# Kernel optimization log

Hardware: AMD Instinct MI355X
Metric: run time of the kernel (lower is better)

Reference implementation:

```python
import jax, jax.numpy as jnp
import numpy as np

DIM = 1024
HEADS = 16
DIM_HEAD = DIM // HEADS  # 64
MAX_FREQ = 256


def rotate_half(x):
    # interleaved pairs: (..., d) -> rotate each (x1, x2) pair to (-x2, x1)
    x = x.reshape(*x.shape[:-1], -1, 2)
    x1, x2 = x[..., 0], x[..., 1]
    return jnp.stack([-x2, x1], axis=-1).reshape(*x.shape[:-2], -1)


def axial_freqs_2d(H, W, rot_dim, max_freq):
    # 'pixel' freqs: linspace(1, max_freq/2, n) * pi per axis; each axis gets rot_dim/2 rotary dims
    n = rot_dim // 4
    freqs = jnp.linspace(1.0, max_freq / 2.0, n, dtype=jnp.float32) * jnp.pi
    ph = jnp.linspace(-1.0, 1.0, H, dtype=jnp.float32)
    pw = jnp.linspace(-1.0, 1.0, W, dtype=jnp.float32)
    fh = jnp.repeat(ph[:, None] * freqs[None, :], 2, axis=-1)  # (H, rot_dim//2)
    fw = jnp.repeat(pw[:, None] * freqs[None, :], 2, axis=-1)  # (W, rot_dim//2)
    fh = jnp.broadcast_to(fh[:, None, :], (H, W, rot_dim // 2))
    fw = jnp.broadcast_to(fw[None, :, :], (H, W, rot_dim // 2))
    return jnp.concatenate([fh, fw], axis=-1)  # (H, W, rot_dim)


def setup_inputs() -> dict:
    key = jax.random.key(0)
    k1, k2, k3 = jax.random.split(key, 3)
    b, H, W = 8, 32, 32
    L = H * W
    x = jax.random.normal(k1, (b, L, DIM), dtype=jnp.float32)
    # torch Linear weights stored pre-transposed for direct x @ W
    w_qkv = jax.random.normal(k2, (DIM, 3 * DIM), dtype=jnp.float32) * (DIM ** -0.5)
    w_proj = jax.random.normal(k3, (DIM, DIM), dtype=jnp.float32) * (DIM ** -0.5)
    return {"x": x, "w_qkv": w_qkv, "w_proj": w_proj, "H": H, "W": W}


def reference(x, w_qkv, w_proj, H, W):
    b, L, d = x.shape
    qkv = x @ w_qkv  # (b, L, 3d)
    q, k, v = jnp.split(qkv, 3, axis=-1)

    def split_heads(t):
        return t.reshape(b, L, HEADS, DIM_HEAD)  # (b, L, h, dh)

    q, k, v = split_heads(q), split_heads(k), split_heads(v)

    # 2D axial RoPE over the full head dim (rope_use_dim == dim_head)
    freqs = axial_freqs_2d(H, W, DIM_HEAD, MAX_FREQ).reshape(L, DIM_HEAD)
    cos = jnp.cos(freqs)[None, :, None, :]  # (1, L, 1, dh)
    sin = jnp.sin(freqs)[None, :, None, :]
    q = q * cos + rotate_half(q) * sin
    k = k * cos + rotate_half(k) * sin

    # module pre-scales q by dh^-0.5 AND SDPA scales again by dh^-0.5 -> dh^-1 total (faithful)
    scale_total = 1.0 / DIM_HEAD
    scores = jnp.einsum('blhd,bmhd->bhlm', q, k) * scale_total  # (b, h, L, L)
    attn = jax.nn.softmax(scores, axis=-1)
    out = jnp.einsum('bhlm,bmhd->blhd', attn, v).reshape(b, L, d)
    return out @ w_proj
```

## Files before the change

### kernel.cpp

```cpp
#include <hip/hip_runtime.h>
#include <hip/hip_bf16.h>
#include <math.h>

typedef __bf16 bf16_t;
typedef __attribute__((ext_vector_type(8))) __bf16 bf16x8;
typedef __attribute__((ext_vector_type(4))) __bf16 bf16x4;
typedef __attribute__((ext_vector_type(4))) short s16x4;
typedef __attribute__((ext_vector_type(4))) float f32x4;

#define AS1C(p) ((const __attribute__((address_space(1))) void*)(p))
#define AS3(p)  ((__attribute__((address_space(3))) void*)(p))

__device__ __forceinline__ float fast_exp2(float x) { return __builtin_amdgcn_exp2f(x); }

__global__ __launch_bounds__(256) void k_cvt(const float* __restrict__ in,
                                             bf16_t* __restrict__ out, int n4) {
    int i = blockIdx.x * 256 + threadIdx.x;
    if (i < n4) {
        float4 v = reinterpret_cast<const float4*>(in)[i];
        bf16x4 o;
        o[0] = (bf16_t)v.x; o[1] = (bf16_t)v.y; o[2] = (bf16_t)v.z; o[3] = (bf16_t)v.w;
        reinterpret_cast<bf16x4*>(out)[i] = o;
    }
}

__global__ __launch_bounds__(256) void k_tconv(const float* __restrict__ in,
                                               bf16_t* __restrict__ out, int R, int C) {
    __shared__ float tile[64][65];
    int r0 = blockIdx.y * 64, c0 = blockIdx.x * 64;
#pragma unroll
    for (int i = 0; i < 16; ++i) {
        int e = i * 256 + threadIdx.x;
        int r = e >> 6, c = e & 63;
        tile[r][c] = in[(size_t)(r0 + r) * C + c0 + c];
    }
    __syncthreads();
#pragma unroll
    for (int i = 0; i < 16; ++i) {
        int e = i * 256 + threadIdx.x;
        int c = e >> 6, r = e & 63;
        out[(size_t)(c0 + c) * R + r0 + r] = (bf16_t)tile[r][c];
    }
}

__global__ __launch_bounds__(256) void k_tab(float* __restrict__ cosT,
                                             float* __restrict__ sinT) {
    int i = blockIdx.x * 256 + threadIdx.x;
    int l = i >> 6, d = i & 63;
    int hh = l >> 5, ww = l & 31;
    float pos = (d < 32) ? (-1.0f + (2.0f / 31.0f) * (float)hh)
                         : (-1.0f + (2.0f / 31.0f) * (float)ww);
    int fi = (d & 31) >> 1;
    float fb = (1.0f + (127.0f / 15.0f) * (float)fi) * 3.14159265358979323846f;
    float fr = pos * fb;
    cosT[i] = cosf(fr);
    sinT[i] = sinf(fr);
}

__device__ __forceinline__ void gemm_core(const bf16_t* __restrict__ A,
                                          const bf16_t* __restrict__ Bt,
                                          int K, int rowA0, int colB0,
                                          int w, int l, bf16_t* As, bf16_t* Bs,
                                          f32x4 acc[4][4]) {
    const int wr = w >> 1, wc = w & 1;
    for (int kt = 0; kt < K; kt += 64) {
#pragma unroll
        for (int i = 0; i < 4; ++i) {
            int rr = (i * 4 + w) * 8 + (l >> 3);
            int ch = (l & 7) * 8;
            __builtin_amdgcn_global_load_lds(AS1C(A + (size_t)(rowA0 + rr) * K + kt + ch),
                                             AS3(As + (i * 4 + w) * 512), 16, 0, 0);
            __builtin_amdgcn_global_load_lds(AS1C(Bt + (size_t)(colB0 + rr) * K + kt + ch),
                                             AS3(Bs + (i * 4 + w) * 512), 16, 0, 0);
        }
        __syncthreads();
#pragma unroll
        for (int kk = 0; kk < 2; ++kk) {
            bf16x8 af[4], bfr[4];
#pragma unroll
            for (int m = 0; m < 4; ++m)
                af[m] = *reinterpret_cast<const bf16x8*>(
                    As + (wr * 64 + m * 16 + (l & 15)) * 64 + kk * 32 + (l >> 4) * 8);
#pragma unroll
            for (int n = 0; n < 4; ++n)
                bfr[n] = *reinterpret_cast<const bf16x8*>(
                    Bs + (wc * 64 + n * 16 + (l & 15)) * 64 + kk * 32 + (l >> 4) * 8);
#pragma unroll
            for (int m = 0; m < 4; ++m)
#pragma unroll
                for (int n = 0; n < 4; ++n)
                    acc[m][n] = __builtin_amdgcn_mfma_f32_16x16x32_bf16(af[m], bfr[n],
                                                                        acc[m][n], 0, 0, 0);
        }
        __syncthreads();
    }
}

__global__ __launch_bounds__(256) void k_gemm_qkv(const bf16_t* __restrict__ A,
                                                  const bf16_t* __restrict__ Bt,
                                                  const float* __restrict__ cosT,
                                                  const float* __restrict__ sinT,
                                                  bf16_t* __restrict__ qb,
                                                  bf16_t* __restrict__ kb,
                                                  bf16_t* __restrict__ vb) {
    __shared__ alignas(128) bf16_t As[128 * 64];
    __shared__ alignas(128) bf16_t Bs[128 * 64];
    const int tid = threadIdx.x, w = tid >> 6, l = tid & 63;
    const int rowA0 = blockIdx.y * 128, colB0 = blockIdx.x * 128;
    f32x4 acc[4][4] = {};
    gemm_core(A, Bt, 1024, rowA0, colB0, w, l, As, Bs, acc);
    const int wr = w >> 1, wc = w & 1;
    const int part = colB0 >> 10;
#pragma unroll
    for (int m = 0; m < 4; ++m) {
#pragma unroll
        for (int n = 0; n < 4; ++n) {
            const int c = colB0 + wc * 64 + n * 16 + (l & 15);
            const int head = (c & 1023) >> 6;
            const int d = c & 63;
            const int rbase = rowA0 + wr * 64 + m * 16 + (l >> 4) * 4;
            if (part == 2) {
#pragma unroll
                for (int r = 0; r < 4; ++r) {
                    int row = rbase + r;
                    int bb = row >> 10, ll = row & 1023;
                    vb[(((size_t)bb * 16 + head) * 64 + d) * 1024 + ll] = (bf16_t)acc[m][n][r];
                }
            } else {
                bf16_t* dst = (part == 0) ? qb : kb;
#pragma unroll
                for (int r = 0; r < 4; ++r) {
                    int row = rbase + r;
                    int bb = row >> 10, ll = row & 1023;
                    float v0 = acc[m][n][r];
                    float vp = __shfl_xor(v0, 1, 64);
                    float cs = cosT[ll * 64 + d];
                    float sn = sinT[ll * 64 + d];
                    float res = (d & 1) ? fmaf(vp, sn, v0 * cs) : fmaf(-vp, sn, v0 * cs);
                    dst[(((size_t)bb * 16 + head) * 1024 + ll) * 64 + d] = (bf16_t)res;
                }
            }
        }
    }
}

__global__ __launch_bounds__(256) void k_gemm_out(const bf16_t* __restrict__ A,
                                                  const bf16_t* __restrict__ Bt,
                                                  float* __restrict__ out) {
    __shared__ alignas(128) bf16_t As[128 * 64];
    __shared__ alignas(128) bf16_t Bs[128 * 64];
    const int tid = threadIdx.x, w = tid >> 6, l = tid & 63;
    const int rowA0 = blockIdx.y * 128, colB0 = blockIdx.x * 128;
    f32x4 acc[4][4] = {};
    gemm_core(A, Bt, 1024, rowA0, colB0, w, l, As, Bs, acc);
    const int wr = w >> 1, wc = w & 1;
#pragma unroll
    for (int m = 0; m < 4; ++m)
#pragma unroll
        for (int n = 0; n < 4; ++n) {
            int c = colB0 + wc * 64 + n * 16 + (l & 15);
            int rbase = rowA0 + wr * 64 + m * 16 + (l >> 4) * 4;
#pragma unroll
            for (int r = 0; r < 4; ++r)
                out[(size_t)(rbase + r) * 1024 + c] = acc[m][n][r];
        }
}

__global__ __launch_bounds__(256, 4) void k_attn(const bf16_t* __restrict__ qb,
                                                 const bf16_t* __restrict__ kb,
                                                 const bf16_t* __restrict__ vb,
                                                 bf16_t* __restrict__ ob) {
    __shared__ alignas(128) bf16_t Ks[2][64 * 64];
    __shared__ alignas(128) bf16_t Vs[2][64 * 64];
    const int tid = threadIdx.x, w = tid >> 6, l = tid & 63;
    const int g = l >> 4;
    const int bid = blockIdx.x;
    const int bs = (bid & 7) * 128 + (bid >> 3);
    const int bh = bs >> 3, bi = bh >> 4, h = bh & 15;
    const int q0 = (bs & 7) * 128;
    const bf16_t* qbase = qb + (size_t)bh * 1024 * 64;
    const bf16_t* kbase = kb + (size_t)bh * 1024 * 64;
    const bf16_t* vbase = vb + (size_t)bh * 64 * 1024;

    bf16x8 qf[2][2];
#pragma unroll
    for (int m = 0; m < 2; ++m) {
        int qrow = q0 + m * 64 + w * 16 + (l & 15);
#pragma unroll
        for (int kk = 0; kk < 2; ++kk)
            qf[m][kk] = *reinterpret_cast<const bf16x8*>(
                qbase + (size_t)qrow * 64 + kk * 32 + g * 8);
    }

    float m_run[2] = {-1e30f, -1e30f};
    float l_run[2] = {0.f, 0.f};
    f32x4 o_acc[2][4] = {};

    const int srow = l >> 3;
    const int sc = 8 * ((l & 7) ^ srow);
#define STAGE(buf, kv0)                                                                   \
    {                                                                                     \
        _Pragma("unroll")                                                                 \
        for (int i = 0; i < 2; ++i) {                                                     \
            int rr = (i * 4 + w) * 8 + srow;                                              \
            __builtin_amdgcn_global_load_lds(AS1C(kbase + (size_t)((kv0) + rr) * 64 + sc),\
                                             AS3(&Ks[buf][(i * 4 + w) * 512]), 16, 0, 0); \
            __builtin_amdgcn_global_load_lds(AS1C(vbase + (size_t)rr * 1024 + (kv0) + sc),\
                                             AS3(&Vs[buf][(i * 4 + w) * 512]), 16, 0, 0); \
        }                                                                                 \
    }

    STAGE(0, 0);
    __syncthreads();

    const float SCL = 1.4426950408889634f / 64.0f;
    int cur = 0;
    for (int t = 0; t < 16; ++t) {
        if (t < 15) STAGE(cur ^ 1, (t + 1) * 64);

        f32x4 sacc[2][4] = {};
#pragma unroll
        for (int kk = 0; kk < 2; ++kk)
#pragma unroll
            for (int n = 0; n < 4; ++n) {
                int rr = n * 16 + (l & 15);
                int ec = (kk * 32 + g * 8) ^ ((l & 7) << 3);
                bf16x8 kfr = *reinterpret_cast<const bf16x8*>(&Ks[cur][rr * 64 + ec]);
                sacc[0][n] = __builtin_amdgcn_mfma_f32_16x16x32_bf16(kfr, qf[0][kk], sacc[0][n], 0, 0, 0);
                sacc[1][n] = __builtin_amdgcn_mfma_f32_16x16x32_bf16(kfr, qf[1][kk], sacc[1][n], 0, 0, 0);
            }

        s16x4 pa[2][4];
#pragma unroll
        for (int m = 0; m < 2; ++m) {
            float mxr = -1e30f;
#pragma unroll
            for (int n = 0; n < 4; ++n)
#pragma unroll
                for (int r = 0; r < 4; ++r) mxr = fmaxf(mxr, sacc[m][n][r]);
            mxr = fmaxf(mxr, __shfl_xor(mxr, 16, 64));
            mxr = fmaxf(mxr, __shfl_xor(mxr, 32, 64));
            float mx = mxr * SCL;
            float mo = m_run[m];
            if (__any(mx > mo + 8.0f)) {
                float mn = fmaxf(mo, mx);
                float corr = fast_exp2(mo - mn);
                l_run[m] *= corr;
                m_run[m] = mn; mo = mn;
#pragma unroll
                for (int r = 0; r < 4; ++r) {
                    float c2 = __shfl(corr, (l & 48) | (g * 4 + r), 64);
#pragma unroll
                    for (int n = 0; n < 4; ++n) o_acc[m][n][r] *= c2;
                }
            }
            float lsum = 0.f;
#pragma unroll
            for (int n = 0; n < 4; ++n) {
                bf16x4 pb;
#pragma unroll
                for (int r = 0; r < 4; ++r) {
                    float pv = fast_exp2(fmaf(sacc[m][n][r], SCL, -mo));
                    lsum += pv;
                    pb[r] = (bf16_t)pv;
                }
                pa[m][n] = __builtin_bit_cast(s16x4, pb);
            }
            l_run[m] += lsum;
        }

        const char* vrow = (const char*)&Vs[cur][0] + (l & 15) * 128;
#pragma unroll
        for (int c = 0; c < 4; ++c) {
            int kvb = (c * 32 + g * 8) ^ ((l & 7) << 4);
#pragma unroll
            for (int nd = 0; nd < 4; ++nd) {
                s16x4 vf = *reinterpret_cast<const s16x4*>(vrow + nd * 2048 + kvb);
                o_acc[0][nd] = __builtin_amdgcn_mfma_f32_16x16x16bf16_1k(pa[0][c], vf, o_acc[0][nd], 0, 0, 0);
                o_acc[1][nd] = __builtin_amdgcn_mfma_f32_16x16x16bf16_1k(pa[1][c], vf, o_acc[1][nd], 0, 0, 0);
            }
        }
        __syncthreads();
        cur ^= 1;
    }

#pragma unroll
    for (int m = 0; m < 2; ++m) {
        float ls = l_run[m];
        ls += __shfl_xor(ls, 16, 64);
        ls += __shfl_xor(ls, 32, 64);
        float inv = 1.0f / ls;
#pragma unroll
        for (int r = 0; r < 4; ++r) {
            float c2 = __shfl(inv, (l & 48) | (g * 4 + r), 64);
            int row = q0 + m * 64 + w * 16 + g * 4 + r;
#pragma unroll
            for (int n = 0; n < 4; ++n)
                ob[((size_t)bi * 1024 + row) * 1024 + h * 64 + n * 16 + (l & 15)] =
                    (bf16_t)(o_acc[m][n][r] * c2);
        }
    }
#undef STAGE
}

extern "C" void kernel_launch(void* const* d_in, const int* in_sizes, int n_in,
                              void* d_out, int out_size, void* d_ws, size_t ws_size,
                              hipStream_t stream) {
    (void)in_sizes; (void)n_in; (void)out_size; (void)ws_size;
    const float* x     = (const float*)d_in[0];
    const float* wqkv  = (const float*)d_in[1];
    const float* wproj = (const float*)d_in[2];
    char* ws = (char*)d_ws;

    bf16_t* xb  = (bf16_t*)(ws);
    bf16_t* wqT = (bf16_t*)(ws + 16777216ull);
    bf16_t* wpT = (bf16_t*)(ws + 23068672ull);
    bf16_t* qb  = (bf16_t*)(ws + 25165824ull);
    bf16_t* kb  = (bf16_t*)(ws + 41943040ull);
    bf16_t* vb  = (bf16_t*)(ws + 58720256ull);
    bf16_t* ob  = (bf16_t*)(ws + 75497472ull);
    float*  cosT = (float*)(ws + 92274688ull);
    float*  sinT = (float*)(ws + 92536832ull);

    k_cvt<<<8192, 256, 0, stream>>>(x, xb, 2097152);
    k_tconv<<<dim3(48, 16), 256, 0, stream>>>(wqkv, wqT, 1024, 3072);
    k_tconv<<<dim3(16, 16), 256, 0, stream>>>(wproj, wpT, 1024, 1024);
    k_tab<<<256, 256, 0, stream>>>(cosT, sinT);
    k_gemm_qkv<<<dim3(24, 64), 256, 0, stream>>>(xb, wqT, cosT, sinT, qb, kb, vb);
    k_attn<<<1024, 256, 0, stream>>>(qb, kb, vb, ob);
    k_gemm_out<<<dim3(8, 64), 256, 0, stream>>>(ob, wpT, (float*)d_out);
}
```

Baseline: 188.8 us.

## Rewrite QKV GEMM with 256x256 tiles, double-buffered LDS, swizzled layout

The QKV projection GEMM moves from 128x128 tiles on 256 threads to 256x256 tiles on 512 threads (8 waves, each computing 128x64). It also double-buffers shared memory with direct global-to-LDS loads, applies an XOR swizzle to avoid bank conflicts, remaps block IDs for L2 locality, and raises wave priority around the MFMA bursts. The aim is better data reuse and hiding global load latency behind matrix compute. In exchange it uses 128 KB of LDS per block and more accumulator registers per thread, and the grid shrinks to 384 blocks.

New measurement: 186.6 us. No clear change (-1.2%).

```diff
diff --git a/kernel.cpp b/kernel.cpp
--- a/kernel.cpp
+++ b/kernel.cpp
@@ -96,29 +96,103 @@
     }
 }
 
-__global__ __launch_bounds__(256) void k_gemm_qkv(const bf16_t* __restrict__ A,
-                                                  const bf16_t* __restrict__ Bt,
-                                                  const float* __restrict__ cosT,
-                                                  const float* __restrict__ sinT,
-                                                  bf16_t* __restrict__ qb,
-                                                  bf16_t* __restrict__ kb,
-                                                  bf16_t* __restrict__ vb) {
-    __shared__ alignas(128) bf16_t As[128 * 64];
-    __shared__ alignas(128) bf16_t Bs[128 * 64];
+__global__ __launch_bounds__(512, 2) void k_gemm_qkv(const bf16_t* __restrict__ A,
+                                                     const bf16_t* __restrict__ Bt,
+                                                     const float* __restrict__ cosT,
+                                                     const float* __restrict__ sinT,
+                                                     bf16_t* __restrict__ qb,
+                                                     bf16_t* __restrict__ kb,
+                                                     bf16_t* __restrict__ vb) {
+    __shared__ alignas(128) bf16_t As[2][256 * 64];
+    __shared__ alignas(128) bf16_t Bs[2][256 * 64];
     const int tid = threadIdx.x, w = tid >> 6, l = tid & 63;
-    const int rowA0 = blockIdx.y * 128, colB0 = blockIdx.x * 128;
-    f32x4 acc[4][4] = {};
-    gemm_core(A, Bt, 1024, rowA0, colB0, w, l, As, Bs, acc);
-    const int wr = w >> 1, wc = w & 1;
+    const int wr = w >> 2, wc = w & 3;
+    const int bid = blockIdx.x;
+    const int sw = (bid & 7) * 48 + (bid >> 3);
+    const int bx = sw % 12, by = sw / 12;
+    const int rowA0 = by * 256, colB0 = bx * 256;
+    const int sc = ((l & 7) ^ (l >> 3)) << 3;
+
+    f32x4 acc[8][4] = {};
+
+#define STG(dA, dB, kt)                                                                     \
+    {                                                                                       \
+        _Pragma("unroll")                                                                   \
+        for (int j = 0; j < 4; ++j) {                                                       \
+            int rr = j * 64 + w * 8 + (l >> 3);                                             \
+            __builtin_amdgcn_global_load_lds(                                               \
+                AS1C(A + (size_t)(rowA0 + rr) * 1024 + (kt) * 64 + sc),                     \
+                AS3((dA) + (j * 64 + w * 8) * 64), 16, 0, 0);                               \
+            __builtin_amdgcn_global_load_lds(                                               \
+                AS1C(Bt + (size_t)(colB0 + rr) * 1024 + (kt) * 64 + sc),                    \
+                AS3((dB) + (j * 64 + w * 8) * 64), 16, 0, 0);                               \
+        }                                                                                   \
+    }
+
+    STG(&As[0][0], &Bs[0][0], 0);
+
+    for (int T = 0; T < 16; ++T) {
+        bf16_t* cA = &As[T & 1][0];
+        bf16_t* cB = &Bs[T & 1][0];
+        if (T < 15) {
+            STG(&As[(T & 1) ^ 1][0], &Bs[(T & 1) ^ 1][0], T + 1);
+            asm volatile("s_waitcnt vmcnt(8)" ::: "memory");
+        } else {
+            asm volatile("s_waitcnt vmcnt(0)" ::: "memory");
+        }
+        __builtin_amdgcn_s_barrier();
+
+#pragma unroll
+        for (int kk = 0; kk < 2; ++kk) {
+            const int ec = (kk * 32 + (l >> 4) * 8) ^ ((l & 7) << 3);
+            bf16x8 af[4], bfr[4];
+#pragma unroll
+            for (int n = 0; n < 4; ++n)
+                bfr[n] = *reinterpret_cast<const bf16x8*>(
+                    cB + (wc * 64 + n * 16 + (l & 15)) * 64 + ec);
+#pragma unroll
+            for (int mm = 0; mm < 4; ++mm)
+                af[mm] = *reinterpret_cast<const bf16x8*>(
+                    cA + (wr * 128 + mm * 16 + (l & 15)) * 64 + ec);
+            asm volatile("s_waitcnt lgkmcnt(0)" ::: "memory");
+            __builtin_amdgcn_sched_barrier(0);
+            __builtin_amdgcn_s_setprio(1);
+#pragma unroll
+            for (int mm = 0; mm < 4; ++mm)
+#pragma unroll
+                for (int n = 0; n < 4; ++n)
+                    acc[mm][n] = __builtin_amdgcn_mfma_f32_16x16x32_bf16(af[mm], bfr[n],
+                                                                         acc[mm][n], 0, 0, 0);
+            __builtin_amdgcn_s_setprio(0);
+            __builtin_amdgcn_s_barrier();
+#pragma unroll
+            for (int mm = 0; mm < 4; ++mm)
+                af[mm] = *reinterpret_cast<const bf16x8*>(
+                    cA + (wr * 128 + (4 + mm) * 16 + (l & 15)) * 64 + ec);
+            asm volatile("s_waitcnt lgkmcnt(0)" ::: "memory");
+            __builtin_amdgcn_sched_barrier(0);
+            __builtin_amdgcn_s_setprio(1);
+#pragma unroll
+            for (int mm = 0; mm < 4; ++mm)
+#pragma unroll
+                for (int n = 0; n < 4; ++n)
+                    acc[4 + mm][n] = __builtin_amdgcn_mfma_f32_16x16x32_bf16(af[mm], bfr[n],
+                                                                             acc[4 + mm][n], 0, 0, 0);
+            __builtin_amdgcn_s_setprio(0);
+            __builtin_amdgcn_s_barrier();
+        }
+    }
+#undef STG
+
     const int part = colB0 >> 10;
 #pragma unroll
-    for (int m = 0; m < 4; ++m) {
+    for (int m = 0; m < 8; ++m) {
 #pragma unroll
         for (int n = 0; n < 4; ++n) {
             const int c = colB0 + wc * 64 + n * 16 + (l & 15);
             const int head = (c & 1023) >> 6;
             const int d = c & 63;
-            const int rbase = rowA0 + wr * 64 + m * 16 + (l >> 4) * 4;
+            const int rbase = rowA0 + wr * 128 + m * 16 + (l >> 4) * 4;
             if (part == 2) {
 #pragma unroll
                 for (int r = 0; r < 4; ++r) {
@@ -326,7 +400,7 @@
     k_tconv<<<dim3(48, 16), 256, 0, stream>>>(wqkv, wqT, 1024, 3072);
     k_tconv<<<dim3(16, 16), 256, 0, stream>>>(wproj, wpT, 1024, 1024);
     k_tab<<<256, 256, 0, stream>>>(cosT, sinT);
-    k_gemm_qkv<<<dim3(24, 64), 256, 0, stream>>>(xb, wqT, cosT, sinT, qb, kb, vb);
+    k_gemm_qkv<<<384, 512, 0, stream>>>(xb, wqT, cosT, sinT, qb, kb, vb);
     k_attn<<<1024, 256, 0, stream>>>(qb, kb, vb, ob);
     k_gemm_out<<<dim3(8, 64), 256, 0, stream>>>(ob, wpT, (float*)d_out);
 }
```

## Double-buffer GEMM LDS loads with XOR swizzle, tile remap, LDS-staged V transpose

Applied to the files above, without the earlier changes.

Reworks the shared GEMM core into a two-stage pipeline. The next K-tile is issued through global_load_lds while MFMAs run on the current one, with explicit vmcnt waits and s_setprio. LDS columns are XOR-swizzled to cut bank conflicts, and blocks are remapped through a 1D grid so neighbouring blocks share tiles in L2. The V epilogue now transposes through LDS and writes 16-byte vectors instead of scattered 2-byte stores. The cost is 64KB of LDS per block, which caps occupancy at two blocks per CU.

New measurement: 162.9 us. -13.7%, faster.

```diff
diff --git a/kernel.cpp b/kernel.cpp
--- a/kernel.cpp
+++ b/kernel.cpp
@@ -57,77 +57,124 @@
     sinT[i] = sinf(fr);
 }
 
-__device__ __forceinline__ void gemm_core(const bf16_t* __restrict__ A,
-                                          const bf16_t* __restrict__ Bt,
-                                          int K, int rowA0, int colB0,
-                                          int w, int l, bf16_t* As, bf16_t* Bs,
-                                          f32x4 acc[4][4]) {
+__device__ __forceinline__ void gemm128_pipe(const bf16_t* __restrict__ A,
+                                             const bf16_t* __restrict__ Bt,
+                                             int rowA0, int colB0, int w, int l,
+                                             bf16_t* As, bf16_t* Bs,
+                                             f32x4 acc[4][4]) {
     const int wr = w >> 1, wc = w & 1;
-    for (int kt = 0; kt < K; kt += 64) {
-#pragma unroll
-        for (int i = 0; i < 4; ++i) {
-            int rr = (i * 4 + w) * 8 + (l >> 3);
-            int ch = (l & 7) * 8;
-            __builtin_amdgcn_global_load_lds(AS1C(A + (size_t)(rowA0 + rr) * K + kt + ch),
-                                             AS3(As + (i * 4 + w) * 512), 16, 0, 0);
-            __builtin_amdgcn_global_load_lds(AS1C(Bt + (size_t)(colB0 + rr) * K + kt + ch),
-                                             AS3(Bs + (i * 4 + w) * 512), 16, 0, 0);
-        }
-        __syncthreads();
+    const int r8 = l >> 3;
+    const int sc = ((l & 7) ^ r8) << 3;
+
+#define STG8(buf, kt)                                                                      \
+    {                                                                                      \
+        _Pragma("unroll")                                                                  \
+        for (int j = 0; j < 4; ++j) {                                                      \
+            int rr = j * 32 + w * 8 + r8;                                                  \
+            __builtin_amdgcn_global_load_lds(                                              \
+                AS1C(A + (size_t)(rowA0 + rr) * 1024 + (kt) * 64 + sc),                    \
+                AS3(As + (buf) * 8192 + (j * 32 + w * 8) * 64), 16, 0, 0);                 \
+            __builtin_amdgcn_global_load_lds(                                              \
+                AS1C(Bt + (size_t)(colB0 + rr) * 1024 + (kt) * 64 + sc),                   \
+                AS3(Bs + (buf) * 8192 + (j * 32 + w * 8) * 64), 16, 0, 0);                 \
+        }                                                                                  \
+    }
+
+    STG8(0, 0);
+    for (int T = 0; T < 16; ++T) {
+        if (T < 15) {
+            STG8((T + 1) & 1, T + 1);
+            asm volatile("s_waitcnt vmcnt(8)" ::: "memory");
+        } else {
+            asm volatile("s_waitcnt vmcnt(0)" ::: "memory");
+        }
+        __builtin_amdgcn_s_barrier();
+        const bf16_t* cA = As + (T & 1) * 8192;
+        const bf16_t* cB = Bs + (T & 1) * 8192;
 #pragma unroll
         for (int kk = 0; kk < 2; ++kk) {
+            const int ec = (kk * 32 + (l >> 4) * 8) ^ ((l & 7) << 3);
             bf16x8 af[4], bfr[4];
 #pragma unroll
-            for (int m = 0; m < 4; ++m)
-                af[m] = *reinterpret_cast<const bf16x8*>(
-                    As + (wr * 64 + m * 16 + (l & 15)) * 64 + kk * 32 + (l >> 4) * 8);
+            for (int mm = 0; mm < 4; ++mm)
+                af[mm] = *reinterpret_cast<const bf16x8*>(
+                    cA + (wr * 64 + mm * 16 + (l & 15)) * 64 + ec);
 #pragma unroll
             for (int n = 0; n < 4; ++n)
                 bfr[n] = *reinterpret_cast<const bf16x8*>(
-                    Bs + (wc * 64 + n * 16 + (l & 15)) * 64 + kk * 32 + (l >> 4) * 8);
-#pragma unroll
-            for (int m = 0; m < 4; ++m)
+                    cB + (wc * 64 + n * 16 + (l & 15)) * 64 + ec);
+            asm volatile("s_waitcnt lgkmcnt(0)" ::: "memory");
+            __builtin_amdgcn_sched_barrier(0);
+            __builtin_amdgcn_s_setprio(1);
+#pragma unroll
+            for (int mm = 0; mm < 4; ++mm)
 #pragma unroll
                 for (int n = 0; n < 4; ++n)
-                    acc[m][n] = __builtin_amdgcn_mfma_f32_16x16x32_bf16(af[m], bfr[n],
-                                                                        acc[m][n], 0, 0, 0);
-        }
+                    acc[mm][n] = __builtin_amdgcn_mfma_f32_16x16x32_bf16(af[mm], bfr[n],
+                                                                         acc[mm][n], 0, 0, 0);
+            __builtin_amdgcn_s_setprio(0);
+        }
+        __builtin_amdgcn_s_barrier();
+    }
+#undef STG8
+}
+
+__global__ __launch_bounds__(256, 2) void k_gemm_qkv(const bf16_t* __restrict__ A,
+                                                     const bf16_t* __restrict__ Bt,
+                                                     const float* __restrict__ cosT,
+                                                     const float* __restrict__ sinT,
+                                                     bf16_t* __restrict__ qb,
+                                                     bf16_t* __restrict__ kb,
+                                                     bf16_t* __restrict__ vb) {
+    __shared__ alignas(128) char smem[65536];
+    bf16_t* As = (bf16_t*)smem;
+    bf16_t* Bs = (bf16_t*)(smem + 32768);
+    const int tid = threadIdx.x, w = tid >> 6, l = tid & 63;
+    const int wr = w >> 1, wc = w & 1;
+    const int bid = blockIdx.x;
+    const int sw = (bid & 7) * 192 + (bid >> 3);
+    const int bx = sw % 24, by = sw / 24;
+    const int rowA0 = by * 128, colB0 = bx * 128;
+
+    f32x4 acc[4][4] = {};
+    gemm128_pipe(A, Bt, rowA0, colB0, w, l, As, Bs, acc);
+
+    const int part = colB0 >> 10;
+    if (part == 2) {
+        __builtin_amdgcn_sched_barrier(0);
         __syncthreads();
-    }
-}
-
-__global__ __launch_bounds__(256) void k_gemm_qkv(const bf16_t* __restrict__ A,
-                                                  const bf16_t* __restrict__ Bt,
-                                                  const float* __restrict__ cosT,
-                                                  const float* __restrict__ sinT,
-                                                  bf16_t* __restrict__ qb,
-                                                  bf16_t* __restrict__ kb,
-                                                  bf16_t* __restrict__ vb) {
-    __shared__ alignas(128) bf16_t As[128 * 64];
-    __shared__ alignas(128) bf16_t Bs[128 * 64];
-    const int tid = threadIdx.x, w = tid >> 6, l = tid & 63;
-    const int rowA0 = blockIdx.y * 128, colB0 = blockIdx.x * 128;
-    f32x4 acc[4][4] = {};
-    gemm_core(A, Bt, 1024, rowA0, colB0, w, l, As, Bs, acc);
-    const int wr = w >> 1, wc = w & 1;
-    const int part = colB0 >> 10;
-#pragma unroll
-    for (int m = 0; m < 4; ++m) {
-#pragma unroll
-        for (int n = 0; n < 4; ++n) {
-            const int c = colB0 + wc * 64 + n * 16 + (l & 15);
-            const int head = (c & 1023) >> 6;
-            const int d = c & 63;
-            const int rbase = rowA0 + wr * 64 + m * 16 + (l >> 4) * 4;
-            if (part == 2) {
-#pragma unroll
-                for (int r = 0; r < 4; ++r) {
-                    int row = rbase + r;
-                    int bb = row >> 10, ll = row & 1023;
-                    vb[(((size_t)bb * 16 + head) * 64 + d) * 1024 + ll] = (bf16_t)acc[m][n][r];
-                }
-            } else {
-                bf16_t* dst = (part == 0) ? qb : kb;
+        bf16_t* Tb = (bf16_t*)smem;
+#pragma unroll
+        for (int m = 0; m < 4; ++m)
+#pragma unroll
+            for (int n = 0; n < 4; ++n) {
+                int cc = wc * 64 + n * 16 + (l & 15);
+                int rr = wr * 64 + m * 16 + (l >> 4) * 4;
+#pragma unroll
+                for (int r = 0; r < 4; ++r)
+                    Tb[cc * 136 + rr + r] = (bf16_t)acc[m][n][r];
+            }
+        __syncthreads();
+        const int j = tid >> 1, half = tid & 1;
+        const int c = colB0 + j;
+        const int head = (c & 1023) >> 6, d = c & 63;
+        const int bb = rowA0 >> 10, ll0 = rowA0 & 1023;
+        bf16_t* dst = vb + (((size_t)bb * 16 + head) * 64 + d) * 1024 + ll0 + half * 64;
+        const bf16_t* srcp = Tb + j * 136 + half * 64;
+#pragma unroll
+        for (int e = 0; e < 8; ++e)
+            *reinterpret_cast<bf16x8*>(dst + e * 8) =
+                *reinterpret_cast<const bf16x8*>(srcp + e * 8);
+    } else {
+        bf16_t* dstb = (part == 0) ? qb : kb;
+#pragma unroll
+        for (int m = 0; m < 4; ++m)
+#pragma unroll
+            for (int n = 0; n < 4; ++n) {
+                const int c = colB0 + wc * 64 + n * 16 + (l & 15);
+                const int head = (c & 1023) >> 6;
+                const int d = c & 63;
+                const int rbase = rowA0 + wr * 64 + m * 16 + (l >> 4) * 4;
 #pragma unroll
                 for (int r = 0; r < 4; ++r) {
                     int row = rbase + r;
@@ -137,23 +184,28 @@
                     float cs = cosT[ll * 64 + d];
                     float sn = sinT[ll * 64 + d];
                     float res = (d & 1) ? fmaf(vp, sn, v0 * cs) : fmaf(-vp, sn, v0 * cs);
-                    dst[(((size_t)bb * 16 + head) * 1024 + ll) * 64 + d] = (bf16_t)res;
+                    dstb[(((size_t)bb * 16 + head) * 1024 + ll) * 64 + d] = (bf16_t)res;
                 }
             }
-        }
-    }
-}
-
-__global__ __launch_bounds__(256) void k_gemm_out(const bf16_t* __restrict__ A,
-                                                  const bf16_t* __restrict__ Bt,
-                                                  float* __restrict__ out) {
-    __shared__ alignas(128) bf16_t As[128 * 64];
-    __shared__ alignas(128) bf16_t Bs[128 * 64];
+    }
+}
+
+__global__ __launch_bounds__(256, 2) void k_gemm_out(const bf16_t* __restrict__ A,
+                                                     const bf16_t* __restrict__ Bt,
+                                                     float* __restrict__ out) {
+    __shared__ alignas(128) char smem[65536];
+    bf16_t* As = (bf16_t*)smem;
+    bf16_t* Bs = (bf16_t*)(smem + 32768);
     const int tid = threadIdx.x, w = tid >> 6, l = tid & 63;
-    const int rowA0 = blockIdx.y * 128, colB0 = blockIdx.x * 128;
+    const int wr = w >> 1, wc = w & 1;
+    const int bid = blockIdx.x;
+    const int sw = (bid & 7) * 64 + (bid >> 3);
+    const int bx = sw & 7, by = sw >> 3;
+    const int rowA0 = by * 128, colB0 = bx * 128;
+
     f32x4 acc[4][4] = {};
-    gemm_core(A, Bt, 1024, rowA0, colB0, w, l, As, Bs, acc);
-    const int wr = w >> 1, wc = w & 1;
+    gemm128_pipe(A, Bt, rowA0, colB0, w, l, As, Bs, acc);
+
 #pragma unroll
     for (int m = 0; m < 4; ++m)
 #pragma unroll
@@ -326,7 +378,7 @@
     k_tconv<<<dim3(48, 16), 256, 0, stream>>>(wqkv, wqT, 1024, 3072);
     k_tconv<<<dim3(16, 16), 256, 0, stream>>>(wproj, wpT, 1024, 1024);
     k_tab<<<256, 256, 0, stream>>>(cosT, sinT);
-    k_gemm_qkv<<<dim3(24, 64), 256, 0, stream>>>(xb, wqT, cosT, sinT, qb, kb, vb);
+    k_gemm_qkv<<<1536, 256, 0, stream>>>(xb, wqT, cosT, sinT, qb, kb, vb);
     k_attn<<<1024, 256, 0, stream>>>(qb, kb, vb, ob);
-    k_gemm_out<<<dim3(8, 64), 256, 0, stream>>>(ob, wpT, (float*)d_out);
-}
+    k_gemm_out<<<512, 256, 0, stream>>>(ob, wpT, (float*)d_out);
+}
```
